# Optimization experiments

Hardware: AMD Instinct MI355X
Metric: run time of the kernel (lower is better)

The kernel has to match this reference:

```python
import jax, jax.numpy as jnp
import numpy as np

N = 100000  # nodes
E = 320000  # edges
G = 64      # graphs in the batch


def setup_inputs() -> dict:
    key = jax.random.key(0)
    ks = jax.random.split(key, 16)
    inp = {
        "x": jax.random.normal(ks[0], (N, 512), dtype=jnp.float32),
        "edge_index": jax.random.randint(ks[1], (2, E), 0, N, dtype=jnp.int64),
        "batch": jnp.sort(jax.random.randint(ks[2], (N,), 0, G, dtype=jnp.int64)),
    }
    # GCNConv weights (in, out) and biases, Glorot-ish scale
    dims = [(512, 256), (256, 128), (128, 64), (64, 32)]
    for i, (din, dout) in enumerate(dims):
        inp[f"w{i+1}"] = jax.random.normal(ks[3 + i], (din, dout), dtype=jnp.float32) / np.sqrt(din)
        inp[f"b{i+1}"] = jnp.zeros((dout,), dtype=jnp.float32)
    inp["lw1"] = jax.random.normal(ks[8], (32, 16), dtype=jnp.float32) / np.sqrt(32.0)
    inp["lb1"] = jnp.zeros((16,), dtype=jnp.float32)
    inp["lw2"] = jax.random.normal(ks[9], (16, 2), dtype=jnp.float32) / np.sqrt(16.0)
    inp["lb2"] = jnpp = jnp.zeros((2,), dtype=jnp.float32)
    return inp


def _gcn_conv(h_in, w, b, src, dst, norm, n):
    # x' = D^-1/2 (A+I) D^-1/2 (X W) + b   (PyG GCNConv default)
    h = h_in @ w                                  # [N, out]
    msg = h[src] * norm[:, None]                  # gather + scale over edges(+self-loops)
    out = jax.ops.segment_sum(msg, dst, num_segments=n)  # scatter-add
    return out + b


def reference(x, edge_index, batch, w1, b1, w2, b2, w3, b3, w4, b4, lw1, lb1, lw2, lb2):
    n = x.shape[0]
    loop = jnp.arange(n, dtype=edge_index.dtype)
    src = jnp.concatenate([edge_index[0], loop])  # add self-loops
    dst = jnp.concatenate([edge_index[1], loop])
    # symmetric normalization: deg counted at dst (col) including self-loops
    deg = jax.ops.segment_sum(jnp.ones_like(dst, dtype=x.dtype), dst, num_segments=n)
    dinv = jnp.where(deg > 0, 1.0 / jnp.sqrt(deg), 0.0)
    norm = dinv[src] * dinv[dst]                  # [E+N]

    h = jax.nn.relu(_gcn_conv(x, w1, b1, src, dst, norm, n))
    h = jax.nn.relu(_gcn_conv(h, w2, b2, src, dst, norm, n))
    h = jax.nn.relu(_gcn_conv(h, w3, b3, src, dst, norm, n))
    h = _gcn_conv(h, w4, b4, src, dst, norm, n)   # [N, 32]

    # global mean pool over graphs
    sums = jax.ops.segment_sum(h, batch, num_segments=G)
    cnt = jax.ops.segment_sum(jnp.ones((n,), dtype=h.dtype), batch, num_segments=G)
    pooled = sums / jnp.maximum(cnt, 1.0)[:, None]  # [G, 32]

    # dropout p=0.8 is identity in eval mode
    out = jax.nn.relu(pooled @ lw1 + lb1) @ lw2 + lb2  # [G, 2]
    return out
```

## Files before the change

### kernel.cpp

```cpp
#include <hip/hip_runtime.h>
#include <cstdint>
#include <cstddef>


typedef __attribute__((ext_vector_type(8))) short s16x8;
typedef __attribute__((ext_vector_type(4))) float f32x4;

__device__ __forceinline__ short2 split2(float f) {
    union { float f; unsigned u; } c; c.f = f;
    short hi = (short)(c.u >> 16);
    union { unsigned u; float f; } h; h.u = c.u & 0xffff0000u;
    union { float f; unsigned u; } r; r.f = f - h.f;
    short lo = (short)(r.u >> 16);
    return make_short2(hi, lo);
}

__device__ __forceinline__ void gload16(const void* g, void* l) {
    __builtin_amdgcn_global_load_lds(
        (const __attribute__((address_space(1))) unsigned int*)g,
        (__attribute__((address_space(3))) unsigned int*)l, 16, 0, 0);
}


__global__ void k_count(const int* __restrict__ dst, int E, int* __restrict__ cnt) {
    int e = blockIdx.x * blockDim.x + threadIdx.x;
    if (e < E) atomicAdd(&cnt[dst[e]], 1);
}

__global__ void k_dinv(const int* __restrict__ cnt, int n, float* __restrict__ dinv) {
    int i = blockIdx.x * blockDim.x + threadIdx.x;
    if (i < n) dinv[i] = rsqrtf((float)(cnt[i] + 1));
}

__global__ void k_scan_sums(const int* __restrict__ cnt, int n, int* __restrict__ bsum) {
    __shared__ int s[256];
    int t = threadIdx.x;
    int base = blockIdx.x * 4096 + t * 16;
    int sum = 0;
#pragma unroll
    for (int j = 0; j < 16; ++j) { int i = base + j; if (i < n) sum += cnt[i]; }
    s[t] = sum;
    __syncthreads();
    for (int off = 128; off > 0; off >>= 1) {
        if (t < off) s[t] += s[t + off];
        __syncthreads();
    }
    if (t == 0) bsum[blockIdx.x] = s[0];
}

__global__ void k_scan_offsets(const int* __restrict__ bsum, int nb,
                               int* __restrict__ boff, int* __restrict__ totalp) {
    int t = threadIdx.x;
    int v = (t < nb) ? bsum[t] : 0;
    int x = v;
    for (int off = 1; off < 64; off <<= 1) {
        int y = __shfl_up(x, off);
        if (t >= off) x += y;
    }
    if (t < nb) boff[t] = x - v;
    if (t == 63) *totalp = x;
}

__global__ void k_scan_final(const int* __restrict__ cnt, int n,
                             const int* __restrict__ boff, int* __restrict__ row_ptr) {
    __shared__ int s[256];
    int t = threadIdx.x;
    int base = blockIdx.x * 4096 + t * 16;
    int v[16]; int sum = 0;
#pragma unroll
    for (int j = 0; j < 16; ++j) { int i = base + j; v[j] = (i < n) ? cnt[i] : 0; sum += v[j]; }
    s[t] = sum;
    __syncthreads();
    for (int off = 1; off < 256; off <<= 1) {
        int y = (t >= off) ? s[t - off] : 0;
        __syncthreads();
        s[t] += y;
        __syncthreads();
    }
    int run = boff[blockIdx.x] + ((t == 0) ? 0 : s[t - 1]);
#pragma unroll
    for (int j = 0; j < 16; ++j) {
        int i = base + j;
        if (i < n) row_ptr[i] = run;
        run += v[j];
    }
}

__global__ void k_fill(const int* __restrict__ src, const int* __restrict__ dst, int E,
                       const int* __restrict__ row_ptr, int* __restrict__ cursor,
                       int* __restrict__ csr_src) {
    int e = blockIdx.x * blockDim.x + threadIdx.x;
    if (e >= E) return;
    int d = dst[e];
    int p = atomicAdd(&cursor[d], 1);
    csr_src[row_ptr[d] + p] = src[e];
}


__global__ void k_split_w(const float* __restrict__ w, int N, int total, int kshift,
                          unsigned short* __restrict__ th, unsigned short* __restrict__ tl) {
    int idx = blockIdx.x * blockDim.x + threadIdx.x;
    if (idx >= total) return;
    int nn = idx >> kshift;
    int k  = idx & ((1 << kshift) - 1);
    short2 p = split2(w[(size_t)k * N + nn]);
    th[idx] = (unsigned short)p.x;
    tl[idx] = (unsigned short)p.y;
}


__global__ __launch_bounds__(256)
void k_gemm1(const float* __restrict__ A32,
             const unsigned short* __restrict__ Bth, const unsigned short* __restrict__ Btl,
             float* __restrict__ C, int M) {
    constexpr int K = 512, KT = 16;
    constexpr int APL = 128 * 64;
    constexpr int ABUF = 2 * APL;
    constexpr int BPL = 128 * 64;
    constexpr int BBUF = 2 * BPL;
    extern __shared__ __attribute__((aligned(16))) char lds[];
    char* aB0 = lds;
    char* aB1 = lds + ABUF;
    char* bB0 = lds + 2 * ABUF;
    char* bB1 = bB0 + BBUF;
    char* bB2 = bB1 + BBUF;
    char* aB[2] = {aB0, aB1};
    char* bB[3] = {bB0, bB1, bB2};

    const int tid  = threadIdx.x;
    const int lane = tid & 63;
    const int w    = tid >> 6;
    const int wm   = w & 1;
    const int wn   = w >> 1;
    const int brow = blockIdx.y * 128;
    const int bcol = blockIdx.x * 128;
    const int l15  = lane & 15;
    const int kb   = (lane >> 4) * 16;

    const int arow  = tid >> 1;
    const int ahalf = tid & 1;
    int ag = brow + arow; if (ag > M - 1) ag = M - 1;
    const float* xrow = A32 + (size_t)ag * K + ahalf * 16;
    const int vq = (arow >> 1) & 3;
    const int q0 = ((2 * ahalf) ^ vq) * 16;
    const int q1 = ((2 * ahalf + 1) ^ vq) * 16;

    f32x4 acc[4][4];
#pragma unroll
    for (int i = 0; i < 4; ++i)
#pragma unroll
        for (int j = 0; j < 4; ++j) acc[i][j] = (f32x4){0.f, 0.f, 0.f, 0.f};

    float4 xr[2][4];

    auto X = [&](int t, int p) {
        const float4* q = (const float4*)(xrow + t * 32);
        xr[p][0] = q[0]; xr[p][1] = q[1]; xr[p][2] = q[2]; xr[p][3] = q[3];
    };
    auto SB = [&](char* bbuf, int t) {
#pragma unroll
        for (int u = 0; u < 4; ++u) {
            int id = w + u * 4;
            int hi = (id < 8) ? 1 : 0;
            int s  = hi ? id : id - 8;
            int p  = s * 64 + lane;
            int kq = (p ^ ((p >> 3) & 3)) & 3;
            int col = p >> 2;
            const unsigned short* gs = (hi ? Bth : Btl) + (size_t)(bcol + col) * K + t * 32 + kq * 8;
            gload16(gs, (hi ? bbuf : bbuf + BPL) + s * 1024);
        }
    };
    auto WA = [&](char* abuf, int p) {
        float v[16] = {xr[p][0].x, xr[p][0].y, xr[p][0].z, xr[p][0].w,
                       xr[p][1].x, xr[p][1].y, xr[p][1].z, xr[p][1].w,
                       xr[p][2].x, xr[p][2].y, xr[p][2].z, xr[p][2].w,
                       xr[p][3].x, xr[p][3].y, xr[p][3].z, xr[p][3].w};
        s16x8 h0, h1, l0, l1;
#pragma unroll
        for (int j = 0; j < 8; ++j) { short2 q = split2(v[j]);     h0[j] = q.x; l0[j] = q.y; }
#pragma unroll
        for (int j = 0; j < 8; ++j) { short2 q = split2(v[8 + j]); h1[j] = q.x; l1[j] = q.y; }
        *(s16x8*)(abuf + arow * 64 + q0)       = h0;
        *(s16x8*)(abuf + arow * 64 + q1)       = h1;
        *(s16x8*)(abuf + APL + arow * 64 + q0) = l0;
        *(s16x8*)(abuf + APL + arow * 64 + q1) = l1;
    };
    auto MM = [&](char* abuf, char* bbuf) {
        char* sAh = abuf;
        char* sAl = abuf + APL;
        char* sBh = bbuf;
        char* sBl = bbuf + BPL;
        s16x8 fah[4], fam[4];
#pragma unroll
        for (int i = 0; i < 4; ++i) {
            int row = wm * 64 + i * 16 + l15;
            int o = row * 64 + (kb ^ (((row >> 1) & 3) << 4));
            fah[i] = *(const s16x8*)(sAh + o);
            fam[i] = *(const s16x8*)(sAl + o);
        }
#pragma unroll
        for (int j = 0; j < 4; ++j) {
            int col = wn * 64 + j * 16 + l15;
            int o = col * 64 + (kb ^ (((col >> 1) & 3) << 4));
            s16x8 fbh = *(const s16x8*)(sBh + o);
            s16x8 fbm = *(const s16x8*)(sBl + o);
#pragma unroll
            for (int i = 0; i < 4; ++i) {
                acc[i][j] = __builtin_amdgcn_mfma_f32_16x16x32_bf16(fah[i], fbh, acc[i][j], 0, 0, 0);
                acc[i][j] = __builtin_amdgcn_mfma_f32_16x16x32_bf16(fam[i], fbh, acc[i][j], 0, 0, 0);
                acc[i][j] = __builtin_amdgcn_mfma_f32_16x16x32_bf16(fah[i], fbm, acc[i][j], 0, 0, 0);
            }
        }
    };

    X(0, 0);
    SB(bB[0], 0);
    X(1, 1);
    SB(bB[1], 1);
    WA(aB[0], 0);

#pragma unroll
    for (int t = 0; t < KT; ++t) {
        if (t + 1 < KT) {
            asm volatile("s_waitcnt vmcnt(8) lgkmcnt(0)" ::: "memory");
        } else {
            asm volatile("s_waitcnt vmcnt(0) lgkmcnt(0)" ::: "memory");
        }
        __builtin_amdgcn_sched_barrier(0);
        __builtin_amdgcn_s_barrier();
        if (t + 2 < KT) {
            X(t + 2, t & 1);
            SB(bB[(t + 2) % 3], t + 2);
        }
        MM(aB[t & 1], bB[t % 3]);
        if (t + 1 < KT) WA(aB[(t + 1) & 1], (t + 1) & 1);
    }

#pragma unroll
    for (int i = 0; i < 4; ++i) {
#pragma unroll
        for (int r = 0; r < 4; ++r) {
            int row = brow + wm * 64 + i * 16 + (lane >> 4) * 4 + r;
            if (row >= M) continue;
#pragma unroll
            for (int j = 0; j < 4; ++j) {
                int col = bcol + wn * 64 + j * 16 + l15;
                C[(size_t)row * 256 + col] = acc[i][j][r];
            }
        }
    }
}


template <int FN>
__global__ __launch_bounds__(256)
void k_gemm(const unsigned short* __restrict__ Ah, const unsigned short* __restrict__ Al,
            const unsigned short* __restrict__ Bth, const unsigned short* __restrict__ Btl,
            float* __restrict__ C, int M, int K, int N) {
    constexpr int FM = 4;
    constexpr int BM = 128;
    constexpr int BN = FN * 32;
    constexpr int ABYTES = BM * 64;
    constexpr int BBYTES = BN * 64;
    constexpr int BUF = 2 * ABYTES + 2 * BBYTES;
    __shared__ char lds[2 * BUF];

    const int tid  = threadIdx.x;
    const int lane = tid & 63;
    const int w    = tid >> 6;
    const int wm   = w & 1;
    const int wn   = w >> 1;
    const int brow = blockIdx.y * BM;
    const int bcol = blockIdx.x * BN;
    const int l15  = lane & 15;
    const int kb   = (lane >> 4) * 16;

    f32x4 acc[FM][FN];
#pragma unroll
    for (int i = 0; i < FM; ++i)
#pragma unroll
        for (int j = 0; j < FN; ++j) acc[i][j] = (f32x4){0.f, 0.f, 0.f, 0.f};

    auto stageA = [&](char* base, int k0) {
#pragma unroll
        for (int u = 0; u < 4; ++u) {
            int id = w + u * 4;
            int hi = (id < 8) ? 1 : 0;
            int s  = hi ? id : id - 8;
            int p  = s * 64 + lane;
            int kq = (p ^ ((p >> 3) & 3)) & 3;
            int row = p >> 2;
            const unsigned short* gs = (hi ? Ah : Al) + (size_t)(brow + row) * K + k0 + kq * 8;
            gload16(gs, base + (hi ? 0 : ABYTES) + s * 1024);
        }
    };
    auto stageB = [&](char* base, int k0) {
        char* sBh = base + 2 * ABYTES;
        char* sBl = sBh + BBYTES;
#pragma unroll
        for (int u = 0; u < BN / 32; ++u) {
            int id = w + u * 4;
            int hi = (id < BN / 16) ? 1 : 0;
            int s  = hi ? id : id - BN / 16;
            int p  = s * 64 + lane;
            int kq = (p ^ ((p >> 3) & 3)) & 3;
            int col = p >> 2;
            const unsigned short* gs = (hi ? Bth : Btl) + (size_t)(bcol + col) * K + k0 + kq * 8;
            gload16(gs, (hi ? sBh : sBl) + s * 1024);
        }
    };

    char* cur = lds;
    char* nxt = lds + BUF;
    stageB(cur, 0);
    stageA(cur, 0);
    __syncthreads();

    const int KT = K / 32;
    for (int t = 0; t < KT; ++t) {
        const int k1 = (t + 1) * 32;
        if (t + 1 < KT) {
            stageB(nxt, k1);
            stageA(nxt, k1);
        }
        {
            char* sAh = cur;
            char* sAl = cur + ABYTES;
            char* sBh = cur + 2 * ABYTES;
            char* sBl = sBh + BBYTES;
            s16x8 fah[FM], fam[FM];
#pragma unroll
            for (int i = 0; i < FM; ++i) {
                int row = wm * 64 + i * 16 + l15;
                int o = row * 64 + (kb ^ (((row >> 1) & 3) << 4));
                fah[i] = *(const s16x8*)(sAh + o);
                fam[i] = *(const s16x8*)(sAl + o);
            }
#pragma unroll
            for (int j = 0; j < FN; ++j) {
                int col = wn * FN * 16 + j * 16 + l15;
                int o = col * 64 + (kb ^ (((col >> 1) & 3) << 4));
                s16x8 fbh = *(const s16x8*)(sBh + o);
                s16x8 fbm = *(const s16x8*)(sBl + o);
#pragma unroll
                for (int i = 0; i < FM; ++i) {
                    acc[i][j] = __builtin_amdgcn_mfma_f32_16x16x32_bf16(fah[i], fbh, acc[i][j], 0, 0, 0);
                    acc[i][j] = __builtin_amdgcn_mfma_f32_16x16x32_bf16(fam[i], fbh, acc[i][j], 0, 0, 0);
                    acc[i][j] = __builtin_amdgcn_mfma_f32_16x16x32_bf16(fah[i], fbm, acc[i][j], 0, 0, 0);
                }
            }
        }
        __syncthreads();
        char* tmp = cur; cur = nxt; nxt = tmp;
    }

#pragma unroll
    for (int i = 0; i < FM; ++i) {
#pragma unroll
        for (int r = 0; r < 4; ++r) {
            int row = brow + wm * 64 + i * 16 + (lane >> 4) * 4 + r;
            if (row >= M) continue;
#pragma unroll
            for (int j = 0; j < FN; ++j) {
                int col = bcol + wn * FN * 16 + j * 16 + l15;
                C[(size_t)row * N + col] = acc[i][j][r];
            }
        }
    }
}


__global__ void k_agg_split(const float4* __restrict__ h, const int* __restrict__ row_ptr,
                            const int* __restrict__ csr_src, const float* __restrict__ dinv,
                            const float* __restrict__ bias,
                            unsigned short* __restrict__ oh, unsigned short* __restrict__ ol,
                            int n, int f_shift) {
    int idx = blockIdx.x * blockDim.x + threadIdx.x;
    int dout4 = 1 << f_shift;
    int total = n << f_shift;
    if (idx >= total) return;
    int i = idx >> f_shift;
    int f = idx & (dout4 - 1);

    float di = dinv[i];
    float4 hv = h[(size_t)i * dout4 + f];
    float4 acc;
    acc.x = hv.x * di; acc.y = hv.y * di; acc.z = hv.z * di; acc.w = hv.w * di;

    int s0 = row_ptr[i], s1 = row_ptr[i + 1];
    for (int e = s0; e < s1; ++e) {
        int s = csr_src[e];
        float ds = dinv[s];
        float4 v = h[(size_t)s * dout4 + f];
        acc.x += v.x * ds; acc.y += v.y * ds; acc.z += v.z * ds; acc.w += v.w * ds;
    }
    const float4* b4 = (const float4*)bias;
    float4 b = b4[f];
    float4 o;
    o.x = fmaxf(acc.x * di + b.x, 0.f);
    o.y = fmaxf(acc.y * di + b.y, 0.f);
    o.z = fmaxf(acc.z * di + b.z, 0.f);
    o.w = fmaxf(acc.w * di + b.w, 0.f);

    short2 p0 = split2(o.x), p1 = split2(o.y), p2 = split2(o.z), p3 = split2(o.w);
    size_t base = ((size_t)i << f_shift << 2) + f * 4;
    *(ushort4*)(oh + base) = make_ushort4((unsigned short)p0.x, (unsigned short)p1.x,
                                          (unsigned short)p2.x, (unsigned short)p3.x);
    *(ushort4*)(ol + base) = make_ushort4((unsigned short)p0.y, (unsigned short)p1.y,
                                          (unsigned short)p2.y, (unsigned short)p3.y);
}


__global__ void k_agg(const float4* __restrict__ h, const int* __restrict__ row_ptr,
                      const int* __restrict__ csr_src, const float* __restrict__ dinv,
                      const float* __restrict__ bias, float4* __restrict__ out,
                      int n, int f_shift) {
    int idx = blockIdx.x * blockDim.x + threadIdx.x;
    int dout4 = 1 << f_shift;
    int total = n << f_shift;
    if (idx >= total) return;
    int i = idx >> f_shift;
    int f = idx & (dout4 - 1);

    float di = dinv[i];
    float4 hv = h[(size_t)i * dout4 + f];
    float4 acc;
    acc.x = hv.x * di; acc.y = hv.y * di; acc.z = hv.z * di; acc.w = hv.w * di;

    int s0 = row_ptr[i], s1 = row_ptr[i + 1];
    for (int e = s0; e < s1; ++e) {
        int s = csr_src[e];
        float ds = dinv[s];
        float4 v = h[(size_t)s * dout4 + f];
        acc.x += v.x * ds; acc.y += v.y * ds; acc.z += v.z * ds; acc.w += v.w * ds;
    }
    const float4* b4 = (const float4*)bias;
    float4 b = b4[f];
    float4 o;
    o.x = acc.x * di + b.x;
    o.y = acc.y * di + b.y;
    o.z = acc.z * di + b.z;
    o.w = acc.w * di + b.w;
    out[(size_t)i * dout4 + f] = o;
}


__global__ void k_pool(const float* __restrict__ h, const int* __restrict__ batch,
                       int n, float* __restrict__ pooled) {
    int g = blockIdx.x;
    int start, end;
    {
        int lo = 0, hi = n;
        while (lo < hi) { int mid = (lo + hi) >> 1; if (batch[mid] < g) lo = mid + 1; else hi = mid; }
        start = lo;
        lo = start; hi = n;
        while (lo < hi) { int mid = (lo + hi) >> 1; if (batch[mid] < g + 1) lo = mid + 1; else hi = mid; }
        end = lo;
    }
    int f = threadIdx.x & 31;
    int sub = threadIdx.x >> 5;
    float s = 0.f;
    for (int i = start + sub; i < end; i += 8) s += h[(size_t)i * 32 + f];
    __shared__ float red[8][32];
    red[sub][f] = s;
    __syncthreads();
    if (sub == 0) {
        float t = 0.f;
#pragma unroll
        for (int k = 0; k < 8; ++k) t += red[k][f];
        int c = end - start;
        pooled[g * 32 + f] = t / (float)(c > 0 ? c : 1);
    }
}


__global__ void k_mlp(const float* __restrict__ pooled, const float* __restrict__ lw1,
                      const float* __restrict__ lb1, const float* __restrict__ lw2,
                      const float* __restrict__ lb2, float* __restrict__ out, int g_count) {
    int g = threadIdx.x;
    if (g >= g_count) return;
    float p[32];
#pragma unroll
    for (int k = 0; k < 32; ++k) p[k] = pooled[g * 32 + k];
    float hmid[16];
#pragma unroll
    for (int j = 0; j < 16; ++j) {
        float s = lb1[j];
#pragma unroll
        for (int k = 0; k < 32; ++k) s += p[k] * lw1[k * 16 + j];
        hmid[j] = fmaxf(s, 0.f);
    }
#pragma unroll
    for (int o = 0; o < 2; ++o) {
        float s = lb2[o];
#pragma unroll
        for (int k = 0; k < 16; ++k) s += hmid[k] * lw2[k * 2 + o];
        out[g * 2 + o] = s;
    }
}


extern "C" void kernel_launch(void* const* d_in, const int* in_sizes, int n_in,
                              void* d_out, int out_size, void* d_ws, size_t ws_size,
                              hipStream_t stream) {
    const float* x     = (const float*)d_in[0];
    const int*   ei    = (const int*)d_in[1];
    const int*   batch = (const int*)d_in[2];
    const float* w1 = (const float*)d_in[3];  const float* b1 = (const float*)d_in[4];
    const float* w2 = (const float*)d_in[5];  const float* b2 = (const float*)d_in[6];
    const float* w3 = (const float*)d_in[7];  const float* b3 = (const float*)d_in[8];
    const float* w4 = (const float*)d_in[9];  const float* b4 = (const float*)d_in[10];
    const float* lw1 = (const float*)d_in[11]; const float* lb1 = (const float*)d_in[12];
    const float* lw2 = (const float*)d_in[13]; const float* lb2 = (const float*)d_in[14];
    float* out = (float*)d_out;

    const int n = in_sizes[0] / 512;
    const int E = in_sizes[1] / 2;
    const int G = 64;

    const int* src = ei;
    const int* dst = ei + E;

    char* ws = (char*)d_ws;
    size_t off = 0;
    auto alloc = [&](size_t bytes) -> void* {
        void* p = ws + off;
        off = (off + bytes + 255) & ~((size_t)255);
        return p;
    };
    float*          bufA = (float*)alloc((size_t)n * 256 * sizeof(float));
    unsigned short* pAh  = (unsigned short*)alloc((size_t)n * 256 * 2);
    unsigned short* pAl  = (unsigned short*)alloc((size_t)n * 256 * 2);
    int*   cnt     = (int*)alloc((size_t)n * sizeof(int));
    int*   row_ptr = (int*)alloc((size_t)(n + 1) * sizeof(int));
    int*   cursor  = (int*)alloc((size_t)n * sizeof(int));
    int*   csr     = (int*)alloc((size_t)E * sizeof(int));
    float* dinv    = (float*)alloc((size_t)n * sizeof(float));
    float* pooled  = (float*)alloc((size_t)G * 32 * sizeof(float));
    int*   bsum    = (int*)alloc(64 * sizeof(int));
    int*   boff    = (int*)alloc(64 * sizeof(int));
    unsigned short* w1h = (unsigned short*)alloc(256 * 512 * 2);
    unsigned short* w1l = (unsigned short*)alloc(256 * 512 * 2);
    unsigned short* w2h = (unsigned short*)alloc(128 * 256 * 2);
    unsigned short* w2l = (unsigned short*)alloc(128 * 256 * 2);
    unsigned short* w3h = (unsigned short*)alloc(64 * 128 * 2);
    unsigned short* w3l = (unsigned short*)alloc(64 * 128 * 2);
    unsigned short* w4h = (unsigned short*)alloc(32 * 64 * 2);
    unsigned short* w4l = (unsigned short*)alloc(32 * 64 * 2);
    float* bufB = (float*)(pAl + (size_t)n * 64);
    (void)ws_size;

    hipFuncSetAttribute((const void*)k_gemm1,
                        hipFuncAttributeMaxDynamicSharedMemorySize, 80 * 1024);

    hipMemsetAsync(cnt, 0, (size_t)n * sizeof(int), stream);
    hipMemsetAsync(cursor, 0, (size_t)n * sizeof(int), stream);

    k_split_w<<<(256 * 512 + 255) / 256, 256, 0, stream>>>(w1, 256, 256 * 512, 9, w1h, w1l);
    k_split_w<<<(128 * 256 + 255) / 256, 256, 0, stream>>>(w2, 128, 128 * 256, 8, w2h, w2l);
    k_split_w<<<(64 * 128 + 255) / 256, 256, 0, stream>>>(w3, 64, 64 * 128, 7, w3h, w3l);
    k_split_w<<<(32 * 64 + 255) / 256, 256, 0, stream>>>(w4, 32, 32 * 64, 6, w4h, w4l);

    const int nscan = (n + 4095) / 4096;
    k_count<<<(E + 255) / 256, 256, 0, stream>>>(dst, E, cnt);
    k_dinv <<<(n + 255) / 256, 256, 0, stream>>>(cnt, n, dinv);
    k_scan_sums   <<<nscan, 256, 0, stream>>>(cnt, n, bsum);
    k_scan_offsets<<<1, 64, 0, stream>>>(bsum, nscan, boff, row_ptr + n);
    k_scan_final  <<<nscan, 256, 0, stream>>>(cnt, n, boff, row_ptr);
    k_fill<<<(E + 255) / 256, 256, 0, stream>>>(src, dst, E, row_ptr, cursor, csr);

    const int gy = (n + 127) / 128;

    k_gemm1<<<dim3(2, gy), 256, 80 * 1024, stream>>>(x, w1h, w1l, bufA, n);
    k_agg_split<<<((size_t)n * 64 + 255) / 256, 256, 0, stream>>>(
        (const float4*)bufA, row_ptr, csr, dinv, b1, pAh, pAl, n, 6);

    k_gemm<4><<<dim3(1, gy), 256, 0, stream>>>(pAh, pAl, w2h, w2l, bufA, n, 256, 128);
    k_agg_split<<<((size_t)n * 32 + 255) / 256, 256, 0, stream>>>(
        (const float4*)bufA, row_ptr, csr, dinv, b2, pAh, pAl, n, 5);

    k_gemm<2><<<dim3(1, gy), 256, 0, stream>>>(pAh, pAl, w3h, w3l, bufA, n, 128, 64);
    k_agg_split<<<((size_t)n * 16 + 255) / 256, 256, 0, stream>>>(
        (const float4*)bufA, row_ptr, csr, dinv, b3, pAh, pAl, n, 4);

    k_gemm<1><<<dim3(1, gy), 256, 0, stream>>>(pAh, pAl, w4h, w4l, bufA, n, 64, 32);
    k_agg<<<((size_t)n * 8 + 255) / 256, 256, 0, stream>>>(
        (const float4*)bufA, row_ptr, csr, dinv, b4, (float4*)bufB, n, 3);

    k_pool<<<G, 256, 0, stream>>>(bufB, batch, n, pooled);
    k_mlp<<<1, 64, 0, stream>>>(pooled, lw1, lb1, lw2, lb2, out, G);
}
```

Before: 512.4 us.

## Replace multi-buffered gemm1 pipeline with single-buffered static LDS loop

Rewrites the first GEMM's main loop to use one A and one B LDS buffer (static 32 KB) instead of double-buffered A and triple-buffered B in 80 KB of dynamic LDS. Synchronization changes from explicit waitcnt plus barrier to two __syncthreads per K tile, and the register prefetch depth drops to one tile. The aim is lower LDS use and higher occupancy, at the cost of losing overlap between global loads and MFMA work.

```diff
diff --git a/kernel.cpp b/kernel.cpp
--- a/kernel.cpp
+++ b/kernel.cpp
@@ -115,17 +115,9 @@
              float* __restrict__ C, int M) {
     constexpr int K = 512, KT = 16;
     constexpr int APL = 128 * 64;
-    constexpr int ABUF = 2 * APL;
     constexpr int BPL = 128 * 64;
-    constexpr int BBUF = 2 * BPL;
-    extern __shared__ __attribute__((aligned(16))) char lds[];
-    char* aB0 = lds;
-    char* aB1 = lds + ABUF;
-    char* bB0 = lds + 2 * ABUF;
-    char* bB1 = bB0 + BBUF;
-    char* bB2 = bB1 + BBUF;
-    char* aB[2] = {aB0, aB1};
-    char* bB[3] = {bB0, bB1, bB2};
+    __shared__ char sA[2 * APL];
+    __shared__ char sB[2 * BPL];
 
     const int tid  = threadIdx.x;
     const int lane = tid & 63;
@@ -151,13 +143,26 @@
 #pragma unroll
         for (int j = 0; j < 4; ++j) acc[i][j] = (f32x4){0.f, 0.f, 0.f, 0.f};
 
-    float4 xr[2][4];
-
-    auto X = [&](int t, int p) {
+    float4 xr0, xr1, xr2, xr3;
+
+    auto X = [&](int t) {
         const float4* q = (const float4*)(xrow + t * 32);
-        xr[p][0] = q[0]; xr[p][1] = q[1]; xr[p][2] = q[2]; xr[p][3] = q[3];
+        xr0 = q[0]; xr1 = q[1]; xr2 = q[2]; xr3 = q[3];
     };
-    auto SB = [&](char* bbuf, int t) {
+    auto WA = [&]() {
+        float v[16] = {xr0.x, xr0.y, xr0.z, xr0.w, xr1.x, xr1.y, xr1.z, xr1.w,
+                       xr2.x, xr2.y, xr2.z, xr2.w, xr3.x, xr3.y, xr3.z, xr3.w};
+        s16x8 h0, h1, l0, l1;
+#pragma unroll
+        for (int j = 0; j < 8; ++j) { short2 q = split2(v[j]);     h0[j] = q.x; l0[j] = q.y; }
+#pragma unroll
+        for (int j = 0; j < 8; ++j) { short2 q = split2(v[8 + j]); h1[j] = q.x; l1[j] = q.y; }
+        *(s16x8*)(sA + arow * 64 + q0)       = h0;
+        *(s16x8*)(sA + arow * 64 + q1)       = h1;
+        *(s16x8*)(sA + APL + arow * 64 + q0) = l0;
+        *(s16x8*)(sA + APL + arow * 64 + q1) = l1;
+    };
+    auto SB = [&](int t) {
 #pragma unroll
         for (int u = 0; u < 4; ++u) {
             int id = w + u * 4;
@@ -167,73 +172,49 @@
             int kq = (p ^ ((p >> 3) & 3)) & 3;
             int col = p >> 2;
             const unsigned short* gs = (hi ? Bth : Btl) + (size_t)(bcol + col) * K + t * 32 + kq * 8;
-            gload16(gs, (hi ? bbuf : bbuf + BPL) + s * 1024);
+            gload16(gs, (hi ? sB : sB + BPL) + s * 1024);
         }
     };
-    auto WA = [&](char* abuf, int p) {
-        float v[16] = {xr[p][0].x, xr[p][0].y, xr[p][0].z, xr[p][0].w,
-                       xr[p][1].x, xr[p][1].y, xr[p][1].z, xr[p][1].w,
-                       xr[p][2].x, xr[p][2].y, xr[p][2].z, xr[p][2].w,
-                       xr[p][3].x, xr[p][3].y, xr[p][3].z, xr[p][3].w};
-        s16x8 h0, h1, l0, l1;
-#pragma unroll
-        for (int j = 0; j < 8; ++j) { short2 q = split2(v[j]);     h0[j] = q.x; l0[j] = q.y; }
-#pragma unroll
-        for (int j = 0; j < 8; ++j) { short2 q = split2(v[8 + j]); h1[j] = q.x; l1[j] = q.y; }
-        *(s16x8*)(abuf + arow * 64 + q0)       = h0;
-        *(s16x8*)(abuf + arow * 64 + q1)       = h1;
-        *(s16x8*)(abuf + APL + arow * 64 + q0) = l0;
-        *(s16x8*)(abuf + APL + arow * 64 + q1) = l1;
-    };
-    auto MM = [&](char* abuf, char* bbuf) {
-        char* sAh = abuf;
-        char* sAl = abuf + APL;
-        char* sBh = bbuf;
-        char* sBl = bbuf + BPL;
-        s16x8 fah[4], fam[4];
-#pragma unroll
-        for (int i = 0; i < 4; ++i) {
-            int row = wm * 64 + i * 16 + l15;
-            int o = row * 64 + (kb ^ (((row >> 1) & 3) << 4));
-            fah[i] = *(const s16x8*)(sAh + o);
-            fam[i] = *(const s16x8*)(sAl + o);
-        }
-#pragma unroll
-        for (int j = 0; j < 4; ++j) {
-            int col = wn * 64 + j * 16 + l15;
-            int o = col * 64 + (kb ^ (((col >> 1) & 3) << 4));
-            s16x8 fbh = *(const s16x8*)(sBh + o);
-            s16x8 fbm = *(const s16x8*)(sBl + o);
+
+    X(0);
+    WA();
+    SB(0);
+
+    for (int t = 0; t < KT; ++t) {
+        __syncthreads();
+        if (t + 1 < KT) X(t + 1);
+
+        {
+            char* sAl = sA + APL;
+            char* sBl = sB + BPL;
+            s16x8 fah[4], fam[4];
 #pragma unroll
             for (int i = 0; i < 4; ++i) {
-                acc[i][j] = __builtin_amdgcn_mfma_f32_16x16x32_bf16(fah[i], fbh, acc[i][j], 0, 0, 0);
-                acc[i][j] = __builtin_amdgcn_mfma_f32_16x16x32_bf16(fam[i], fbh, acc[i][j], 0, 0, 0);
-                acc[i][j] = __builtin_amdgcn_mfma_f32_16x16x32_bf16(fah[i], fbm, acc[i][j], 0, 0, 0);
+                int row = wm * 64 + i * 16 + l15;
+                int o = row * 64 + (kb ^ (((row >> 1) & 3) << 4));
+                fah[i] = *(const s16x8*)(sA + o);
+                fam[i] = *(const s16x8*)(sAl + o);
             }
-        }
-    };
-
-    X(0, 0);
-    SB(bB[0], 0);
-    X(1, 1);
-    SB(bB[1], 1);
-    WA(aB[0], 0);
-
-#pragma unroll
-    for (int t = 0; t < KT; ++t) {
+#pragma unroll
+            for (int j = 0; j < 4; ++j) {
+                int col = wn * 64 + j * 16 + l15;
+                int o = col * 64 + (kb ^ (((col >> 1) & 3) << 4));
+                s16x8 fbh = *(const s16x8*)(sB + o);
+                s16x8 fbm = *(const s16x8*)(sBl + o);
+#pragma unroll
+                for (int i = 0; i < 4; ++i) {
+                    acc[i][j] = __builtin_amdgcn_mfma_f32_16x16x32_bf16(fah[i], fbh, acc[i][j], 0, 0, 0);
+                    acc[i][j] = __builtin_amdgcn_mfma_f32_16x16x32_bf16(fam[i], fbh, acc[i][j], 0, 0, 0);
+                    acc[i][j] = __builtin_amdgcn_mfma_f32_16x16x32_bf16(fah[i], fbm, acc[i][j], 0, 0, 0);
+                }
+            }
+        }
+
+        __syncthreads();
         if (t + 1 < KT) {
-            asm volatile("s_waitcnt vmcnt(8) lgkmcnt(0)" ::: "memory");
-        } else {
-            asm volatile("s_waitcnt vmcnt(0) lgkmcnt(0)" ::: "memory");
-        }
-        __builtin_amdgcn_sched_barrier(0);
-        __builtin_amdgcn_s_barrier();
-        if (t + 2 < KT) {
-            X(t + 2, t & 1);
-            SB(bB[(t + 2) % 3], t + 2);
-        }
-        MM(aB[t & 1], bB[t % 3]);
-        if (t + 1 < KT) WA(aB[(t + 1) & 1], (t + 1) & 1);
+            WA();
+            SB(t + 1);
+        }
     }
 
 #pragma unroll
@@ -550,9 +531,6 @@
     float* bufB = (float*)(pAl + (size_t)n * 64);
     (void)ws_size;
 
-    hipFuncSetAttribute((const void*)k_gemm1,
-                        hipFuncAttributeMaxDynamicSharedMemorySize, 80 * 1024);
-
     hipMemsetAsync(cnt, 0, (size_t)n * sizeof(int), stream);
     hipMemsetAsync(cursor, 0, (size_t)n * sizeof(int), stream);
 
@@ -571,7 +549,7 @@
 
     const int gy = (n + 127) / 128;
 
-    k_gemm1<<<dim3(2, gy), 256, 80 * 1024, stream>>>(x, w1h, w1l, bufA, n);
+    k_gemm1<<<dim3(2, gy), 256, 0, stream>>>(x, w1h, w1l, bufA, n);
     k_agg_split<<<((size_t)n * 64 + 255) / 256, 256, 0, stream>>>(
         (const float4*)bufA, row_ptr, csr, dinv, b1, pAh, pAl, n, 6);
 
```

Measured after the change: 504.8 us. Within noise of the previous version (-1.5%).

## Simplify gemm1 pipeline to double-buffered static LDS and merge weight-split launches

Applied to the files above, without the earlier changes.

Replaces the hand-tuned three-stage B buffer with manual vmcnt waits and dynamic 80KB shared memory by a static double buffer for A and B, with a __syncthreads at the end of each k-step. This cuts LDS use from 80KB to 64KB, which may allow more blocks per CU, but the B global-to-LDS loads now have only one step of lead time before they are consumed. It also merges the four weight-split kernels into one launch to reduce launch overhead. The cursor allocation order is swapped, which has no speed intent.

```diff
diff --git a/kernel.cpp b/kernel.cpp
--- a/kernel.cpp
+++ b/kernel.cpp
@@ -97,15 +97,24 @@
 }
 
 
-__global__ void k_split_w(const float* __restrict__ w, int N, int total, int kshift,
-                          unsigned short* __restrict__ th, unsigned short* __restrict__ tl) {
+__global__ void k_split_w_all(const float* __restrict__ w1, const float* __restrict__ w2,
+                              const float* __restrict__ w3, const float* __restrict__ w4,
+                              unsigned short* __restrict__ w1h, unsigned short* __restrict__ w1l,
+                              unsigned short* __restrict__ w2h, unsigned short* __restrict__ w2l,
+                              unsigned short* __restrict__ w3h, unsigned short* __restrict__ w3l,
+                              unsigned short* __restrict__ w4h, unsigned short* __restrict__ w4l) {
     int idx = blockIdx.x * blockDim.x + threadIdx.x;
-    if (idx >= total) return;
-    int nn = idx >> kshift;
-    int k  = idx & ((1 << kshift) - 1);
+    const float* w; unsigned short *th, *tl; int N, ks, loc;
+    if (idx < 131072)      { w = w1; th = w1h; tl = w1l; N = 256; ks = 9; loc = idx; }
+    else if (idx < 163840) { w = w2; th = w2h; tl = w2l; N = 128; ks = 8; loc = idx - 131072; }
+    else if (idx < 172032) { w = w3; th = w3h; tl = w3l; N = 64;  ks = 7; loc = idx - 163840; }
+    else if (idx < 174080) { w = w4; th = w4h; tl = w4l; N = 32;  ks = 6; loc = idx - 172032; }
+    else return;
+    int nn = loc >> ks;
+    int k  = loc & ((1 << ks) - 1);
     short2 p = split2(w[(size_t)k * N + nn]);
-    th[idx] = (unsigned short)p.x;
-    tl[idx] = (unsigned short)p.y;
+    th[loc] = (unsigned short)p.x;
+    tl[loc] = (unsigned short)p.y;
 }
 
 
@@ -115,17 +124,9 @@
              float* __restrict__ C, int M) {
     constexpr int K = 512, KT = 16;
     constexpr int APL = 128 * 64;
-    constexpr int ABUF = 2 * APL;
     constexpr int BPL = 128 * 64;
-    constexpr int BBUF = 2 * BPL;
-    extern __shared__ __attribute__((aligned(16))) char lds[];
-    char* aB0 = lds;
-    char* aB1 = lds + ABUF;
-    char* bB0 = lds + 2 * ABUF;
-    char* bB1 = bB0 + BBUF;
-    char* bB2 = bB1 + BBUF;
-    char* aB[2] = {aB0, aB1};
-    char* bB[3] = {bB0, bB1, bB2};
+    __shared__ char sA[2][2 * APL];
+    __shared__ char sB[2][2 * BPL];
 
     const int tid  = threadIdx.x;
     const int lane = tid & 63;
@@ -157,6 +158,21 @@
         const float4* q = (const float4*)(xrow + t * 32);
         xr[p][0] = q[0]; xr[p][1] = q[1]; xr[p][2] = q[2]; xr[p][3] = q[3];
     };
+    auto WA = [&](char* abuf, int p) {
+        float v[16] = {xr[p][0].x, xr[p][0].y, xr[p][0].z, xr[p][0].w,
+                       xr[p][1].x, xr[p][1].y, xr[p][1].z, xr[p][1].w,
+                       xr[p][2].x, xr[p][2].y, xr[p][2].z, xr[p][2].w,
+                       xr[p][3].x, xr[p][3].y, xr[p][3].z, xr[p][3].w};
+        s16x8 h0, h1, l0, l1;
+#pragma unroll
+        for (int j = 0; j < 8; ++j) { short2 q = split2(v[j]);     h0[j] = q.x; l0[j] = q.y; }
+#pragma unroll
+        for (int j = 0; j < 8; ++j) { short2 q = split2(v[8 + j]); h1[j] = q.x; l1[j] = q.y; }
+        *(s16x8*)(abuf + arow * 64 + q0)       = h0;
+        *(s16x8*)(abuf + arow * 64 + q1)       = h1;
+        *(s16x8*)(abuf + APL + arow * 64 + q0) = l0;
+        *(s16x8*)(abuf + APL + arow * 64 + q1) = l1;
+    };
     auto SB = [&](char* bbuf, int t) {
 #pragma unroll
         for (int u = 0; u < 4; ++u) {
@@ -170,39 +186,22 @@
             gload16(gs, (hi ? bbuf : bbuf + BPL) + s * 1024);
         }
     };
-    auto WA = [&](char* abuf, int p) {
-        float v[16] = {xr[p][0].x, xr[p][0].y, xr[p][0].z, xr[p][0].w,
-                       xr[p][1].x, xr[p][1].y, xr[p][1].z, xr[p][1].w,
-                       xr[p][2].x, xr[p][2].y, xr[p][2].z, xr[p][2].w,
-                       xr[p][3].x, xr[p][3].y, xr[p][3].z, xr[p][3].w};
-        s16x8 h0, h1, l0, l1;
-#pragma unroll
-        for (int j = 0; j < 8; ++j) { short2 q = split2(v[j]);     h0[j] = q.x; l0[j] = q.y; }
-#pragma unroll
-        for (int j = 0; j < 8; ++j) { short2 q = split2(v[8 + j]); h1[j] = q.x; l1[j] = q.y; }
-        *(s16x8*)(abuf + arow * 64 + q0)       = h0;
-        *(s16x8*)(abuf + arow * 64 + q1)       = h1;
-        *(s16x8*)(abuf + APL + arow * 64 + q0) = l0;
-        *(s16x8*)(abuf + APL + arow * 64 + q1) = l1;
-    };
     auto MM = [&](char* abuf, char* bbuf) {
-        char* sAh = abuf;
         char* sAl = abuf + APL;
-        char* sBh = bbuf;
         char* sBl = bbuf + BPL;
         s16x8 fah[4], fam[4];
 #pragma unroll
         for (int i = 0; i < 4; ++i) {
             int row = wm * 64 + i * 16 + l15;
             int o = row * 64 + (kb ^ (((row >> 1) & 3) << 4));
-            fah[i] = *(const s16x8*)(sAh + o);
+            fah[i] = *(const s16x8*)(abuf + o);
             fam[i] = *(const s16x8*)(sAl + o);
         }
 #pragma unroll
         for (int j = 0; j < 4; ++j) {
             int col = wn * 64 + j * 16 + l15;
             int o = col * 64 + (kb ^ (((col >> 1) & 3) << 4));
-            s16x8 fbh = *(const s16x8*)(sBh + o);
+            s16x8 fbh = *(const s16x8*)(bbuf + o);
             s16x8 fbm = *(const s16x8*)(sBl + o);
 #pragma unroll
             for (int i = 0; i < 4; ++i) {
@@ -214,26 +213,18 @@
     };
 
     X(0, 0);
-    SB(bB[0], 0);
     X(1, 1);
-    SB(bB[1], 1);
-    WA(aB[0], 0);
+    SB(sB[0], 0);
+    WA(sA[0], 0);
+    __syncthreads();
 
 #pragma unroll
     for (int t = 0; t < KT; ++t) {
-        if (t + 1 < KT) {
-            asm volatile("s_waitcnt vmcnt(8) lgkmcnt(0)" ::: "memory");
-        } else {
-            asm volatile("s_waitcnt vmcnt(0) lgkmcnt(0)" ::: "memory");
-        }
-        __builtin_amdgcn_sched_barrier(0);
-        __builtin_amdgcn_s_barrier();
-        if (t + 2 < KT) {
-            X(t + 2, t & 1);
-            SB(bB[(t + 2) % 3], t + 2);
-        }
-        MM(aB[t & 1], bB[t % 3]);
-        if (t + 1 < KT) WA(aB[(t + 1) & 1], (t + 1) & 1);
+        if (t + 2 < KT) X(t + 2, t & 1);
+        if (t + 1 < KT) SB(sB[(t + 1) & 1], t + 1);
+        MM(sA[t & 1], sB[t & 1]);
+        if (t + 1 < KT) WA(sA[(t + 1) & 1], (t + 1) & 1);
+        __syncthreads();
     }
 
 #pragma unroll
@@ -532,8 +523,8 @@
     unsigned short* pAh  = (unsigned short*)alloc((size_t)n * 256 * 2);
     unsigned short* pAl  = (unsigned short*)alloc((size_t)n * 256 * 2);
     int*   cnt     = (int*)alloc((size_t)n * sizeof(int));
+    int*   cursor  = (int*)alloc((size_t)n * sizeof(int));
     int*   row_ptr = (int*)alloc((size_t)(n + 1) * sizeof(int));
-    int*   cursor  = (int*)alloc((size_t)n * sizeof(int));
     int*   csr     = (int*)alloc((size_t)E * sizeof(int));
     float* dinv    = (float*)alloc((size_t)n * sizeof(float));
     float* pooled  = (float*)alloc((size_t)G * 32 * sizeof(float));
@@ -550,16 +541,11 @@
     float* bufB = (float*)(pAl + (size_t)n * 64);
     (void)ws_size;
 
-    hipFuncSetAttribute((const void*)k_gemm1,
-                        hipFuncAttributeMaxDynamicSharedMemorySize, 80 * 1024);
-
     hipMemsetAsync(cnt, 0, (size_t)n * sizeof(int), stream);
     hipMemsetAsync(cursor, 0, (size_t)n * sizeof(int), stream);
 
-    k_split_w<<<(256 * 512 + 255) / 256, 256, 0, stream>>>(w1, 256, 256 * 512, 9, w1h, w1l);
-    k_split_w<<<(128 * 256 + 255) / 256, 256, 0, stream>>>(w2, 128, 128 * 256, 8, w2h, w2l);
-    k_split_w<<<(64 * 128 + 255) / 256, 256, 0, stream>>>(w3, 64, 64 * 128, 7, w3h, w3l);
-    k_split_w<<<(32 * 64 + 255) / 256, 256, 0, stream>>>(w4, 32, 32 * 64, 6, w4h, w4l);
+    k_split_w_all<<<(174080 + 255) / 256, 256, 0, stream>>>(
+        w1, w2, w3, w4, w1h, w1l, w2h, w2l, w3h, w3l, w4h, w4l);
 
     const int nscan = (n + 4095) / 4096;
     k_count<<<(E + 255) / 256, 256, 0, stream>>>(dst, E, cnt);
@@ -571,7 +557,7 @@
 
     const int gy = (n + 127) / 128;
 
-    k_gemm1<<<dim3(2, gy), 256, 80 * 1024, stream>>>(x, w1h, w1l, bufA, n);
+    k_gemm1<<<dim3(2, gy), 256, 0, stream>>>(x, w1h, w1l, bufA, n);
     k_agg_split<<<((size_t)n * 64 + 255) / 256, 256, 0, stream>>>(
         (const float4*)bufA, row_ptr, csr, dinv, b1, pAh, pAl, n, 6);
 
```

Measured after the change: 497.8 us. -2.8%, faster.
